# Performance work log

Measured on AMD Instinct MI355X. Metric: run time of the kernel, lower is better.

Reference implementation:

```python
import jax, jax.numpy as jnp
import numpy as np
from jax import lax

B, S, H, I, E, K = 4, 4096, 1024, 3584, 8, 2


def setup_inputs() -> dict:
    key = jax.random.key(0)
    ks = jax.random.split(key, 5)
    scale_h = 1.0 / np.sqrt(H)
    scale_i = 1.0 / np.sqrt(I)
    return {
        "hidden_states": jax.random.normal(ks[0], (B, S, H), dtype=jnp.float32),
        "gate_w": jax.random.normal(ks[1], (E, H), dtype=jnp.float32) * scale_h,
        "w1": jax.random.normal(ks[2], (E, H, I), dtype=jnp.float32) * scale_h,
        "w3": jax.random.normal(ks[3], (E, H, I), dtype=jnp.float32) * scale_h,
        "w2": jax.random.normal(ks[4], (E, I, H), dtype=jnp.float32) * scale_i,
        "top_k": K,
    }


def reference(hidden_states, gate_w, w1, w3, w2, top_k):
    b, s, h = hidden_states.shape
    n_experts = gate_w.shape[0]
    x = hidden_states.reshape(-1, h)  # [T, H]

    # Router: softmax in fp32, top-k, renormalize (Mixtral style)
    logits = x @ gate_w.T  # [T, E]
    probs = jax.nn.softmax(logits.astype(jnp.float32), axis=-1)
    top_w, top_idx = lax.top_k(probs, top_k)  # [T, K]
    top_w = top_w.astype(x.dtype)
    top_w = top_w / jnp.sum(top_w, axis=-1, keepdims=True)

    # Per-token, per-expert combine weight: [T, E]
    one_hot = jax.nn.one_hot(top_idx, n_experts, dtype=x.dtype)  # [T, K, E]
    w_full = jnp.einsum("tk,tke->te", top_w, one_hot)

    out = jnp.zeros_like(x)
    for e in range(n_experts):  # fixed small loop over experts
        hidden = jax.nn.silu(x @ w1[e]) * (x @ w3[e])  # SwiGLU, [T, I]
        y = hidden @ w2[e]  # [T, H]
        out = out + y * w_full[:, e:e + 1]
    return out.reshape(b, s, h)
```

## Files before the change

kernel.cpp:

```cpp
#include <hip/hip_runtime.h>
#include <hip/hip_bf16.h>

#define T_TOK 16384
#define H_DIM 1024
#define I_DIM 3584
#define E_NUM 8
#define TOTP  32768

typedef __attribute__((ext_vector_type(8))) short s16x8;
typedef __attribute__((ext_vector_type(4))) float f32x4;
typedef unsigned short u16;

__device__ __forceinline__ u16 f2bf(float f) {
    union { float f; unsigned u; } c; c.f = f;
    unsigned r = c.u + 0x7fffu + ((c.u >> 16) & 1u);
    return (u16)(r >> 16);
}

__device__ __forceinline__ void glds16(const u16* g, u16* l) {
    __builtin_amdgcn_global_load_lds(
        (const __attribute__((address_space(1))) unsigned int*)g,
        (__attribute__((address_space(3))) unsigned int*)l,
        16, 0, 0);
}

__global__ __launch_bounds__(64)
void router_k(const float* __restrict__ x, const float* __restrict__ gw,
              int* __restrict__ tk_idx, float* __restrict__ tk_w,
              int* __restrict__ counts, u16* __restrict__ xb)
{
    int t = blockIdx.x;
    int lane = threadIdx.x;
    const float* xr = x + (size_t)t * H_DIM;
    float xv[16];
#pragma unroll
    for (int j = 0; j < 16; j++) xv[j] = xr[j * 64 + lane];
    u16* xo = xb + (size_t)t * H_DIM;
#pragma unroll
    for (int j = 0; j < 16; j++) xo[j * 64 + lane] = f2bf(xv[j]);
    float lg[E_NUM];
#pragma unroll
    for (int e = 0; e < E_NUM; e++) {
        const float* g = gw + e * H_DIM;
        float s = 0.f;
#pragma unroll
        for (int j = 0; j < 16; j++) s += xv[j] * g[j * 64 + lane];
#pragma unroll
        for (int off = 32; off > 0; off >>= 1) s += __shfl_xor(s, off, 64);
        lg[e] = s;
    }
    if (lane == 0) {
        int i1 = 0; float m1 = lg[0];
#pragma unroll
        for (int e = 1; e < E_NUM; e++) if (lg[e] > m1) { m1 = lg[e]; i1 = e; }
        int i2 = -1; float m2 = -3.4e38f;
#pragma unroll
        for (int e = 0; e < E_NUM; e++) if (e != i1 && lg[e] > m2) { m2 = lg[e]; i2 = e; }
        float p1 = 1.f / (1.f + __expf(m2 - m1));
        float p2 = 1.f - p1;
        tk_idx[t * 2]     = i1;
        tk_idx[t * 2 + 1] = i2;
        tk_w[t * 2]       = p1;
        tk_w[t * 2 + 1]   = p2;
        atomicAdd(&counts[i1], 1);
        atomicAdd(&counts[i2], 1);
    }
}

__global__ void offsets_k(const int* __restrict__ counts, int* __restrict__ offsets,
                          int* __restrict__ cursor)
{
    if (threadIdx.x == 0 && blockIdx.x == 0) {
        int acc = 0;
        for (int e = 0; e < E_NUM; e++) { offsets[e] = acc; cursor[e] = acc; acc += counts[e]; }
        offsets[E_NUM] = acc;
    }
}

__global__ __launch_bounds__(256)
void scatter_k(const int* __restrict__ tk_idx, const float* __restrict__ tk_w,
               int* __restrict__ cursor, int* __restrict__ perm, float* __restrict__ pw,
               int* __restrict__ posmap)
{
    int t = blockIdx.x * 256 + threadIdx.x;
    if (t >= T_TOK) return;
#pragma unroll
    for (int k = 0; k < 2; k++) {
        int e = tk_idx[t * 2 + k];
        int pos = atomicAdd(&cursor[e], 1);
        perm[pos] = t;
        pw[pos]   = tk_w[t * 2 + k];
        posmap[t * 2 + k] = pos;
    }
}

__global__ __launch_bounds__(256)
void tcvt_k(const float* __restrict__ src, u16* __restrict__ dst, int M, int N)
{
    size_t eo = (size_t)blockIdx.z * M * N;
    __shared__ u16 tl[32][33];
    int t = threadIdx.x;
    int r = t >> 3, c = (t & 7) * 4;
    int m0 = blockIdx.y * 32, n0 = blockIdx.x * 32;
    float4 v = *reinterpret_cast<const float4*>(src + eo + (size_t)(m0 + r) * N + n0 + c);
    tl[c + 0][r] = f2bf(v.x); tl[c + 1][r] = f2bf(v.y);
    tl[c + 2][r] = f2bf(v.z); tl[c + 3][r] = f2bf(v.w);
    __syncthreads();
    union { u16 s[4]; unsigned long long v; } u;
    u.s[0] = tl[r][c]; u.s[1] = tl[r][c + 1]; u.s[2] = tl[r][c + 2]; u.s[3] = tl[r][c + 3];
    *reinterpret_cast<unsigned long long*>(dst + eo + (size_t)(n0 + r) * M + m0 + c) = u.v;
}

__global__ __launch_bounds__(256, 2)
void gemm1_k(const u16* __restrict__ xb, const u16* __restrict__ w1t,
             const u16* __restrict__ w3t, const int* __restrict__ offsets,
             const int* __restrict__ perm, const float* __restrict__ pw,
             u16* __restrict__ hidden)
{
    int e = blockIdx.z;
    int base = offsets[e];
    int cnt  = offsets[e + 1] - base;
    int m0 = blockIdx.y * 128;
    if (m0 >= cnt) return;
    int n0 = blockIdx.x * 64;

    __shared__ u16 As[128 * 32];
    __shared__ u16 B1s[64 * 32];
    __shared__ u16 B3s[64 * 32];

    int t = threadIdx.x;
    int lane = t & 63, wave = t >> 6;
    int wm = (wave >> 1) * 64, wn = (wave & 1) * 32;
    int l15 = lane & 15, quad = lane >> 4;

    int sr = t >> 2;
    int sc = (t & 3) * 8;
    int p0 = m0 + sr;      if (p0 > cnt - 1) p0 = cnt - 1;
    int p1 = m0 + 64 + sr; if (p1 > cnt - 1) p1 = cnt - 1;
    const u16* a0p = xb + (size_t)perm[base + p0] * H_DIM + sc;
    const u16* a1p = xb + (size_t)perm[base + p1] * H_DIM + sc;
    const u16* b1p = w1t + (size_t)e * I_DIM * H_DIM + (size_t)(n0 + sr) * H_DIM + sc;
    const u16* b3p = w3t + (size_t)e * I_DIM * H_DIM + (size_t)(n0 + sr) * H_DIM + sc;

    u16* As0 = As + t * 8;
    u16* As1 = As + 2048 + t * 8;
    u16* B1d = B1s + t * 8;
    u16* B3d = B3s + t * 8;

    f32x4 acc1[4][2] = {};
    f32x4 acc3[4][2] = {};

    for (int k0 = 0; k0 < H_DIM; k0 += 32) {
        glds16(a0p + k0, As0);
        glds16(a1p + k0, As1);
        glds16(b1p + k0, B1d);
        glds16(b3p + k0, B3d);
        __syncthreads();
        s16x8 af[4];
#pragma unroll
        for (int i = 0; i < 4; i++)
            af[i] = *reinterpret_cast<const s16x8*>(As + (wm + i * 16 + l15) * 32 + quad * 8);
#pragma unroll
        for (int j = 0; j < 2; j++) {
            s16x8 b1 = *reinterpret_cast<const s16x8*>(B1s + (wn + j * 16 + l15) * 32 + quad * 8);
            s16x8 b3 = *reinterpret_cast<const s16x8*>(B3s + (wn + j * 16 + l15) * 32 + quad * 8);
#pragma unroll
            for (int i = 0; i < 4; i++) {
                acc1[i][j] = __builtin_amdgcn_mfma_f32_16x16x32_bf16(af[i], b1, acc1[i][j], 0, 0, 0);
                acc3[i][j] = __builtin_amdgcn_mfma_f32_16x16x32_bf16(af[i], b3, acc3[i][j], 0, 0, 0);
            }
        }
        __syncthreads();
    }

#pragma unroll
    for (int i = 0; i < 4; i++) {
#pragma unroll
        for (int j = 0; j < 2; j++) {
            int col = n0 + wn + j * 16 + l15;
#pragma unroll
            for (int r = 0; r < 4; r++) {
                int p = m0 + wm + i * 16 + quad * 4 + r;
                if (p < cnt) {
                    float z1 = acc1[i][j][r];
                    float z3 = acc3[i][j][r];
                    float hv = (z1 / (1.f + __expf(-z1))) * z3 * pw[base + p];
                    hidden[(size_t)(base + p) * I_DIM + col] = f2bf(hv);
                }
            }
        }
    }
}

__global__ __launch_bounds__(256, 2)
void gemm2_k(const u16* __restrict__ hidden, const u16* __restrict__ w2t,
             const int* __restrict__ offsets, float* __restrict__ ybuf)
{
    int e = blockIdx.z;
    int base = offsets[e];
    int cnt  = offsets[e + 1] - base;
    int m0 = blockIdx.y * 128;
    if (m0 >= cnt) return;
    int n0 = blockIdx.x * 128;

    __shared__ u16 As[128 * 32];
    __shared__ u16 Bs[128 * 32];

    int t = threadIdx.x;
    int lane = t & 63, wave = t >> 6;
    int wm = (wave >> 1) * 64, wn = (wave & 1) * 64;
    int l15 = lane & 15, quad = lane >> 4;

    int sr = t >> 2;
    int sc = (t & 3) * 8;
    int p0 = m0 + sr;      if (p0 > cnt - 1) p0 = cnt - 1;
    int p1 = m0 + 64 + sr; if (p1 > cnt - 1) p1 = cnt - 1;
    const u16* a0p = hidden + (size_t)(base + p0) * I_DIM + sc;
    const u16* a1p = hidden + (size_t)(base + p1) * I_DIM + sc;
    const u16* wb  = w2t + (size_t)e * H_DIM * I_DIM;
    const u16* b0p = wb + (size_t)(n0 + sr) * I_DIM + sc;
    const u16* b1p = wb + (size_t)(n0 + 64 + sr) * I_DIM + sc;

    u16* As0 = As + t * 8;
    u16* As1 = As + 2048 + t * 8;
    u16* Bs0 = Bs + t * 8;
    u16* Bs1 = Bs + 2048 + t * 8;

    f32x4 acc[4][4] = {};

    for (int k0 = 0; k0 < I_DIM; k0 += 32) {
        glds16(a0p + k0, As0);
        glds16(a1p + k0, As1);
        glds16(b0p + k0, Bs0);
        glds16(b1p + k0, Bs1);
        __syncthreads();
        s16x8 af[4];
#pragma unroll
        for (int i = 0; i < 4; i++)
            af[i] = *reinterpret_cast<const s16x8*>(As + (wm + i * 16 + l15) * 32 + quad * 8);
#pragma unroll
        for (int j = 0; j < 4; j++) {
            s16x8 bfv = *reinterpret_cast<const s16x8*>(Bs + (wn + j * 16 + l15) * 32 + quad * 8);
#pragma unroll
            for (int i = 0; i < 4; i++)
                acc[i][j] = __builtin_amdgcn_mfma_f32_16x16x32_bf16(af[i], bfv, acc[i][j], 0, 0, 0);
        }
        __syncthreads();
    }

#pragma unroll
    for (int i = 0; i < 4; i++) {
#pragma unroll
        for (int r = 0; r < 4; r++) {
            int p = m0 + wm + i * 16 + quad * 4 + r;
            if (p < cnt) {
                float* orow = ybuf + (size_t)(base + p) * H_DIM + n0 + wn;
#pragma unroll
                for (int j = 0; j < 4; j++)
                    orow[j * 16 + l15] = acc[i][j][r];
            }
        }
    }
}

__global__ __launch_bounds__(256)
void combine_k(const float* __restrict__ ybuf, const int* __restrict__ posmap,
               float* __restrict__ out)
{
    int t = blockIdx.x;
    int c = threadIdx.x * 4;
    int pa = posmap[t * 2];
    int pb = posmap[t * 2 + 1];
    float4 a = *reinterpret_cast<const float4*>(ybuf + (size_t)pa * H_DIM + c);
    float4 b = *reinterpret_cast<const float4*>(ybuf + (size_t)pb * H_DIM + c);
    float4 o = make_float4(a.x + b.x, a.y + b.y, a.z + b.z, a.w + b.w);
    *reinterpret_cast<float4*>(out + (size_t)t * H_DIM + c) = o;
}

extern "C" void kernel_launch(void* const* d_in, const int* in_sizes, int n_in,
                              void* d_out, int out_size, void* d_ws, size_t ws_size,
                              hipStream_t stream)
{
    (void)in_sizes; (void)n_in; (void)ws_size; (void)out_size;
    const float* x  = (const float*)d_in[0];
    const float* gw = (const float*)d_in[1];
    const float* w1 = (const float*)d_in[2];
    const float* w3 = (const float*)d_in[3];
    const float* w2 = (const float*)d_in[4];
    float* out = (float*)d_out;

    char* ws = (char*)d_ws;
    int*   counts  = (int*)ws;
    int*   offsets = counts + 8;
    int*   cursor  = offsets + 9;
    int*   tk_idx  = (int*)(ws + 128);
    float* tk_w    = (float*)(ws + 128 + 131072);
    int*   perm    = (int*)(ws + 128 + 2 * 131072);
    float* pw      = (float*)(ws + 128 + 3 * 131072);
    int*   posmap  = (int*)(ws + 128 + 4 * 131072);
    u16* xb     = (u16*)(ws + (1 << 20));
    u16* w1t    = xb + 16777216ull;
    u16* w3t    = w1t + 29360128ull;
    u16* w2t    = w3t + 29360128ull;
    u16* hidden = w2t + 29360128ull;
    float* ybuf = (float*)(ws + (1 << 20));

    hipMemsetAsync(ws, 0, 128, stream);
    router_k<<<T_TOK, 64, 0, stream>>>(x, gw, tk_idx, tk_w, counts, xb);
    offsets_k<<<1, 64, 0, stream>>>(counts, offsets, cursor);
    scatter_k<<<T_TOK / 256, 256, 0, stream>>>(tk_idx, tk_w, cursor, perm, pw, posmap);
    tcvt_k<<<dim3(I_DIM / 32, H_DIM / 32, E_NUM), 256, 0, stream>>>(w1, w1t, H_DIM, I_DIM);
    tcvt_k<<<dim3(I_DIM / 32, H_DIM / 32, E_NUM), 256, 0, stream>>>(w3, w3t, H_DIM, I_DIM);
    tcvt_k<<<dim3(H_DIM / 32, I_DIM / 32, E_NUM), 256, 0, stream>>>(w2, w2t, I_DIM, H_DIM);
    gemm1_k<<<dim3(I_DIM / 64, 128, E_NUM), 256, 0, stream>>>(xb, w1t, w3t, offsets, perm, pw, hidden);
    gemm2_k<<<dim3(H_DIM / 128, 128, E_NUM), 256, 0, stream>>>(hidden, w2t, offsets, ybuf);
    combine_k<<<T_TOK, 256, 0, stream>>>(ybuf, posmap, out);
}
```

Before: 1.906 ms.

## Enlarge GEMM tiles to 256x256x64 with double-buffered LDS, swizzle and interleaved w1/w3

Both expert GEMMs move from 128-row tiles with 32-wide K steps to 256x256 tiles with 64-wide K steps and 512 threads. LDS is double-buffered so the next K tile's global-to-LDS loads overlap the MFMAs, with XOR-swizzled LDS addressing and s_setprio around the MFMA blocks. w1 and w3 are packed into one interleaved transposed matrix, so gemm1 reads a single B operand whose adjacent 16-column groups hold matching gate and up outputs. This is meant to raise arithmetic intensity and hide load latency, at the cost of 128KB LDS per block, many more accumulator registers, and more wasted work on the last partial row tile of each expert.

```diff
diff --git a/kernel.cpp b/kernel.cpp
--- a/kernel.cpp
+++ b/kernel.cpp
@@ -5,6 +5,7 @@
 #define H_DIM 1024
 #define I_DIM 3584
 #define E_NUM 8
+#define N13   7168
 #define TOTP  32768
 
 typedef __attribute__((ext_vector_type(8))) short s16x8;
@@ -111,153 +112,244 @@
     *reinterpret_cast<unsigned long long*>(dst + eo + (size_t)(n0 + r) * M + m0 + c) = u.v;
 }
 
-__global__ __launch_bounds__(256, 2)
-void gemm1_k(const u16* __restrict__ xb, const u16* __restrict__ w1t,
-             const u16* __restrict__ w3t, const int* __restrict__ offsets,
-             const int* __restrict__ perm, const float* __restrict__ pw,
-             u16* __restrict__ hidden)
+__global__ __launch_bounds__(256)
+void tcvt13_k(const float* __restrict__ src, u16* __restrict__ dst, int mat)
+{
+    size_t eo_s = (size_t)blockIdx.z * H_DIM * I_DIM;
+    size_t eo_d = (size_t)blockIdx.z * (size_t)N13 * H_DIM;
+    __shared__ u16 tl[32][33];
+    int t = threadIdx.x;
+    int r = t >> 3, c = (t & 7) * 4;
+    int m0 = blockIdx.y * 32, n0 = blockIdx.x * 32;
+    float4 v = *reinterpret_cast<const float4*>(src + eo_s + (size_t)(m0 + r) * I_DIM + n0 + c);
+    tl[c + 0][r] = f2bf(v.x); tl[c + 1][r] = f2bf(v.y);
+    tl[c + 2][r] = f2bf(v.z); tl[c + 3][r] = f2bf(v.w);
+    __syncthreads();
+    union { u16 s[4]; unsigned long long v; } u;
+    u.s[0] = tl[r][c]; u.s[1] = tl[r][c + 1]; u.s[2] = tl[r][c + 2]; u.s[3] = tl[r][c + 3];
+    int ic = n0 + r;
+    int orow = ((ic >> 4) << 5) + (mat << 4) + (ic & 15);
+    *reinterpret_cast<unsigned long long*>(dst + eo_d + (size_t)orow * H_DIM + m0 + c) = u.v;
+}
+
+
+__global__ __launch_bounds__(512, 2)
+void gemm1_k(const u16* __restrict__ xb, const u16* __restrict__ w13t,
+             const int* __restrict__ offsets, const int* __restrict__ perm,
+             const float* __restrict__ pw, u16* __restrict__ hidden)
 {
     int e = blockIdx.z;
     int base = offsets[e];
     int cnt  = offsets[e + 1] - base;
-    int m0 = blockIdx.y * 128;
+    int m0 = blockIdx.y * 256;
     if (m0 >= cnt) return;
-    int n0 = blockIdx.x * 64;
-
-    __shared__ u16 As[128 * 32];
-    __shared__ u16 B1s[64 * 32];
-    __shared__ u16 B3s[64 * 32];
+    int n0 = blockIdx.x * 256;
+
+    __shared__ u16 As[2][256 * 64];
+    __shared__ u16 Bs[2][256 * 64];
 
     int t = threadIdx.x;
     int lane = t & 63, wave = t >> 6;
-    int wm = (wave >> 1) * 64, wn = (wave & 1) * 32;
+    int wm = (wave >> 2) * 128;
+    int wn = (wave & 3) * 64;
     int l15 = lane & 15, quad = lane >> 4;
-
-    int sr = t >> 2;
-    int sc = (t & 3) * 8;
-    int p0 = m0 + sr;      if (p0 > cnt - 1) p0 = cnt - 1;
-    int p1 = m0 + 64 + sr; if (p1 > cnt - 1) p1 = cnt - 1;
-    const u16* a0p = xb + (size_t)perm[base + p0] * H_DIM + sc;
-    const u16* a1p = xb + (size_t)perm[base + p1] * H_DIM + sc;
-    const u16* b1p = w1t + (size_t)e * I_DIM * H_DIM + (size_t)(n0 + sr) * H_DIM + sc;
-    const u16* b3p = w3t + (size_t)e * I_DIM * H_DIM + (size_t)(n0 + sr) * H_DIM + sc;
-
-    u16* As0 = As + t * 8;
-    u16* As1 = As + 2048 + t * 8;
-    u16* B1d = B1s + t * 8;
-    u16* B3d = B3s + t * 8;
-
-    f32x4 acc1[4][2] = {};
-    f32x4 acc3[4][2] = {};
-
-    for (int k0 = 0; k0 < H_DIM; k0 += 32) {
-        glds16(a0p + k0, As0);
-        glds16(a1p + k0, As1);
-        glds16(b1p + k0, B1d);
-        glds16(b3p + k0, B3d);
-        __syncthreads();
-        s16x8 af[4];
-#pragma unroll
-        for (int i = 0; i < 4; i++)
-            af[i] = *reinterpret_cast<const s16x8*>(As + (wm + i * 16 + l15) * 32 + quad * 8);
-#pragma unroll
-        for (int j = 0; j < 2; j++) {
-            s16x8 b1 = *reinterpret_cast<const s16x8*>(B1s + (wn + j * 16 + l15) * 32 + quad * 8);
-            s16x8 b3 = *reinterpret_cast<const s16x8*>(B3s + (wn + j * 16 + l15) * 32 + quad * 8);
+    int x7 = l15 & 7;
+    int s0 = (quad ^ x7) * 8;
+    int s1 = ((4 + quad) ^ x7) * 8;
+
+    int sr = t >> 3;
+    int ss = t & 7;
+    const u16* aptr[4];
+    const u16* bptr[4];
+#pragma unroll
+    for (int l = 0; l < 4; l++) {
+        int ra = l * 64 + sr;
+        int pr = m0 + ra; if (pr > cnt - 1) pr = cnt - 1;
+        aptr[l] = xb + (size_t)perm[base + pr] * H_DIM + (ss ^ (ra & 7)) * 8;
+        bptr[l] = w13t + (size_t)e * N13 * H_DIM + (size_t)(n0 + ra) * H_DIM + (ss ^ (ra & 7)) * 8;
+    }
+
+    auto STAGE = [&](int buf, int k0) {
+#pragma unroll
+        for (int l = 0; l < 4; l++) glds16(aptr[l] + k0, &As[buf][l * 4096 + t * 8]);
+#pragma unroll
+        for (int l = 0; l < 4; l++) glds16(bptr[l] + k0, &Bs[buf][l * 4096 + t * 8]);
+    };
+
+    f32x4 acc[8][4] = {};
+    const int NT = H_DIM / 64;
+
+    STAGE(0, 0);
+    for (int kt = 0; kt < NT; ++kt) {
+        int cur = kt & 1;
+        if (kt + 1 < NT) {
+            STAGE(cur ^ 1, (kt + 1) * 64);
+            asm volatile("s_waitcnt vmcnt(8)" ::: "memory");
+        } else {
+            asm volatile("s_waitcnt vmcnt(0)" ::: "memory");
+        }
+        __builtin_amdgcn_s_barrier();
+        asm volatile("" ::: "memory");
+        const u16* Ab = As[cur];
+        const u16* Bb = Bs[cur];
+#pragma unroll
+        for (int mh = 0; mh < 2; mh++)
+#pragma unroll
+        for (int nh = 0; nh < 2; nh++) {
+            s16x8 af[4][2], bf[2][2];
 #pragma unroll
             for (int i = 0; i < 4; i++) {
-                acc1[i][j] = __builtin_amdgcn_mfma_f32_16x16x32_bf16(af[i], b1, acc1[i][j], 0, 0, 0);
-                acc3[i][j] = __builtin_amdgcn_mfma_f32_16x16x32_bf16(af[i], b3, acc3[i][j], 0, 0, 0);
-            }
-        }
-        __syncthreads();
-    }
-
-#pragma unroll
-    for (int i = 0; i < 4; i++) {
-#pragma unroll
-        for (int j = 0; j < 2; j++) {
-            int col = n0 + wn + j * 16 + l15;
-#pragma unroll
-            for (int r = 0; r < 4; r++) {
-                int p = m0 + wm + i * 16 + quad * 4 + r;
-                if (p < cnt) {
-                    float z1 = acc1[i][j][r];
-                    float z3 = acc3[i][j][r];
-                    float hv = (z1 / (1.f + __expf(-z1))) * z3 * pw[base + p];
-                    hidden[(size_t)(base + p) * I_DIM + col] = f2bf(hv);
+                int row = wm + mh * 64 + i * 16 + l15;
+                af[i][0] = *reinterpret_cast<const s16x8*>(Ab + row * 64 + s0);
+                af[i][1] = *reinterpret_cast<const s16x8*>(Ab + row * 64 + s1);
+            }
+#pragma unroll
+            for (int j = 0; j < 2; j++) {
+                int row = wn + nh * 32 + j * 16 + l15;
+                bf[j][0] = *reinterpret_cast<const s16x8*>(Bb + row * 64 + s0);
+                bf[j][1] = *reinterpret_cast<const s16x8*>(Bb + row * 64 + s1);
+            }
+            __builtin_amdgcn_s_setprio(1);
+#pragma unroll
+            for (int j = 0; j < 2; j++)
+#pragma unroll
+            for (int i = 0; i < 4; i++)
+#pragma unroll
+            for (int kk = 0; kk < 2; kk++)
+                acc[mh * 4 + i][nh * 2 + j] = __builtin_amdgcn_mfma_f32_16x16x32_bf16(
+                    af[i][kk], bf[j][kk], acc[mh * 4 + i][nh * 2 + j], 0, 0, 0);
+            __builtin_amdgcn_s_setprio(0);
+        }
+        __builtin_amdgcn_s_barrier();
+        asm volatile("" ::: "memory");
+    }
+
+    int hc0 = (n0 + wn) >> 1;
+#pragma unroll
+    for (int i = 0; i < 8; i++) {
+        int rowoff = (i >> 2) * 64 + (i & 3) * 16 + quad * 4;
+#pragma unroll
+        for (int r = 0; r < 4; r++) {
+            int p = m0 + wm + rowoff + r;
+            if (p < cnt) {
+                float w = pw[base + p];
+                u16* hrow = hidden + (size_t)(base + p) * I_DIM + hc0;
+#pragma unroll
+                for (int nh = 0; nh < 2; nh++) {
+                    float z1 = acc[i][nh * 2 + 0][r];
+                    float z3 = acc[i][nh * 2 + 1][r];
+                    float hv = (z1 / (1.f + __expf(-z1))) * z3 * w;
+                    hrow[nh * 16 + l15] = f2bf(hv);
                 }
             }
         }
     }
 }
 
-__global__ __launch_bounds__(256, 2)
+__global__ __launch_bounds__(512, 2)
 void gemm2_k(const u16* __restrict__ hidden, const u16* __restrict__ w2t,
              const int* __restrict__ offsets, float* __restrict__ ybuf)
 {
     int e = blockIdx.z;
     int base = offsets[e];
     int cnt  = offsets[e + 1] - base;
-    int m0 = blockIdx.y * 128;
+    int m0 = blockIdx.y * 256;
     if (m0 >= cnt) return;
-    int n0 = blockIdx.x * 128;
-
-    __shared__ u16 As[128 * 32];
-    __shared__ u16 Bs[128 * 32];
+    int n0 = blockIdx.x * 256;
+
+    __shared__ u16 As[2][256 * 64];
+    __shared__ u16 Bs[2][256 * 64];
 
     int t = threadIdx.x;
     int lane = t & 63, wave = t >> 6;
-    int wm = (wave >> 1) * 64, wn = (wave & 1) * 64;
+    int wm = (wave >> 2) * 128;
+    int wn = (wave & 3) * 64;
     int l15 = lane & 15, quad = lane >> 4;
-
-    int sr = t >> 2;
-    int sc = (t & 3) * 8;
-    int p0 = m0 + sr;      if (p0 > cnt - 1) p0 = cnt - 1;
-    int p1 = m0 + 64 + sr; if (p1 > cnt - 1) p1 = cnt - 1;
-    const u16* a0p = hidden + (size_t)(base + p0) * I_DIM + sc;
-    const u16* a1p = hidden + (size_t)(base + p1) * I_DIM + sc;
-    const u16* wb  = w2t + (size_t)e * H_DIM * I_DIM;
-    const u16* b0p = wb + (size_t)(n0 + sr) * I_DIM + sc;
-    const u16* b1p = wb + (size_t)(n0 + 64 + sr) * I_DIM + sc;
-
-    u16* As0 = As + t * 8;
-    u16* As1 = As + 2048 + t * 8;
-    u16* Bs0 = Bs + t * 8;
-    u16* Bs1 = Bs + 2048 + t * 8;
-
-    f32x4 acc[4][4] = {};
-
-    for (int k0 = 0; k0 < I_DIM; k0 += 32) {
-        glds16(a0p + k0, As0);
-        glds16(a1p + k0, As1);
-        glds16(b0p + k0, Bs0);
-        glds16(b1p + k0, Bs1);
-        __syncthreads();
-        s16x8 af[4];
-#pragma unroll
-        for (int i = 0; i < 4; i++)
-            af[i] = *reinterpret_cast<const s16x8*>(As + (wm + i * 16 + l15) * 32 + quad * 8);
-#pragma unroll
-        for (int j = 0; j < 4; j++) {
-            s16x8 bfv = *reinterpret_cast<const s16x8*>(Bs + (wn + j * 16 + l15) * 32 + quad * 8);
+    int x7 = l15 & 7;
+    int s0 = (quad ^ x7) * 8;
+    int s1 = ((4 + quad) ^ x7) * 8;
+
+    int sr = t >> 3;
+    int ss = t & 7;
+    const u16* aptr[4];
+    const u16* bptr[4];
+    const u16* wb = w2t + (size_t)e * H_DIM * I_DIM;
+#pragma unroll
+    for (int l = 0; l < 4; l++) {
+        int ra = l * 64 + sr;
+        int pr = m0 + ra; if (pr > cnt - 1) pr = cnt - 1;
+        aptr[l] = hidden + (size_t)(base + pr) * I_DIM + (ss ^ (ra & 7)) * 8;
+        bptr[l] = wb + (size_t)(n0 + ra) * I_DIM + (ss ^ (ra & 7)) * 8;
+    }
+
+    auto STAGE = [&](int buf, int k0) {
+#pragma unroll
+        for (int l = 0; l < 4; l++) glds16(aptr[l] + k0, &As[buf][l * 4096 + t * 8]);
+#pragma unroll
+        for (int l = 0; l < 4; l++) glds16(bptr[l] + k0, &Bs[buf][l * 4096 + t * 8]);
+    };
+
+    f32x4 acc[8][4] = {};
+    const int NT = I_DIM / 64;
+
+    STAGE(0, 0);
+    for (int kt = 0; kt < NT; ++kt) {
+        int cur = kt & 1;
+        if (kt + 1 < NT) {
+            STAGE(cur ^ 1, (kt + 1) * 64);
+            asm volatile("s_waitcnt vmcnt(8)" ::: "memory");
+        } else {
+            asm volatile("s_waitcnt vmcnt(0)" ::: "memory");
+        }
+        __builtin_amdgcn_s_barrier();
+        asm volatile("" ::: "memory");
+        const u16* Ab = As[cur];
+        const u16* Bb = Bs[cur];
+#pragma unroll
+        for (int mh = 0; mh < 2; mh++)
+#pragma unroll
+        for (int nh = 0; nh < 2; nh++) {
+            s16x8 af[4][2], bf[2][2];
+#pragma unroll
+            for (int i = 0; i < 4; i++) {
+                int row = wm + mh * 64 + i * 16 + l15;
+                af[i][0] = *reinterpret_cast<const s16x8*>(Ab + row * 64 + s0);
+                af[i][1] = *reinterpret_cast<const s16x8*>(Ab + row * 64 + s1);
+            }
+#pragma unroll
+            for (int j = 0; j < 2; j++) {
+                int row = wn + nh * 32 + j * 16 + l15;
+                bf[j][0] = *reinterpret_cast<const s16x8*>(Bb + row * 64 + s0);
+                bf[j][1] = *reinterpret_cast<const s16x8*>(Bb + row * 64 + s1);
+            }
+            __builtin_amdgcn_s_setprio(1);
+#pragma unroll
+            for (int j = 0; j < 2; j++)
 #pragma unroll
             for (int i = 0; i < 4; i++)
-                acc[i][j] = __builtin_amdgcn_mfma_f32_16x16x32_bf16(af[i], bfv, acc[i][j], 0, 0, 0);
-        }
-        __syncthreads();
-    }
-
-#pragma unroll
-    for (int i = 0; i < 4; i++) {
+#pragma unroll
+            for (int kk = 0; kk < 2; kk++)
+                acc[mh * 4 + i][nh * 2 + j] = __builtin_amdgcn_mfma_f32_16x16x32_bf16(
+                    af[i][kk], bf[j][kk], acc[mh * 4 + i][nh * 2 + j], 0, 0, 0);
+            __builtin_amdgcn_s_setprio(0);
+        }
+        __builtin_amdgcn_s_barrier();
+        asm volatile("" ::: "memory");
+    }
+
+#pragma unroll
+    for (int i = 0; i < 8; i++) {
+        int rowoff = (i >> 2) * 64 + (i & 3) * 16 + quad * 4;
 #pragma unroll
         for (int r = 0; r < 4; r++) {
-            int p = m0 + wm + i * 16 + quad * 4 + r;
+            int p = m0 + wm + rowoff + r;
             if (p < cnt) {
                 float* orow = ybuf + (size_t)(base + p) * H_DIM + n0 + wn;
 #pragma unroll
-                for (int j = 0; j < 4; j++)
-                    orow[j * 16 + l15] = acc[i][j][r];
+                for (int nh = 0; nh < 2; nh++)
+#pragma unroll
+                for (int j = 0; j < 2; j++)
+                    orow[nh * 32 + j * 16 + l15] = acc[i][nh * 2 + j][r];
             }
         }
     }
@@ -299,9 +391,8 @@
     float* pw      = (float*)(ws + 128 + 3 * 131072);
     int*   posmap  = (int*)(ws + 128 + 4 * 131072);
     u16* xb     = (u16*)(ws + (1 << 20));
-    u16* w1t    = xb + 16777216ull;
-    u16* w3t    = w1t + 29360128ull;
-    u16* w2t    = w3t + 29360128ull;
+    u16* w13t   = xb + 16777216ull;
+    u16* w2t    = w13t + 58720256ull;
     u16* hidden = w2t + 29360128ull;
     float* ybuf = (float*)(ws + (1 << 20));
 
@@ -309,10 +400,10 @@
     router_k<<<T_TOK, 64, 0, stream>>>(x, gw, tk_idx, tk_w, counts, xb);
     offsets_k<<<1, 64, 0, stream>>>(counts, offsets, cursor);
     scatter_k<<<T_TOK / 256, 256, 0, stream>>>(tk_idx, tk_w, cursor, perm, pw, posmap);
-    tcvt_k<<<dim3(I_DIM / 32, H_DIM / 32, E_NUM), 256, 0, stream>>>(w1, w1t, H_DIM, I_DIM);
-    tcvt_k<<<dim3(I_DIM / 32, H_DIM / 32, E_NUM), 256, 0, stream>>>(w3, w3t, H_DIM, I_DIM);
+    tcvt13_k<<<dim3(I_DIM / 32, H_DIM / 32, E_NUM), 256, 0, stream>>>(w1, w13t, 0);
+    tcvt13_k<<<dim3(I_DIM / 32, H_DIM / 32, E_NUM), 256, 0, stream>>>(w3, w13t, 1);
     tcvt_k<<<dim3(H_DIM / 32, I_DIM / 32, E_NUM), 256, 0, stream>>>(w2, w2t, I_DIM, H_DIM);
-    gemm1_k<<<dim3(I_DIM / 64, 128, E_NUM), 256, 0, stream>>>(xb, w1t, w3t, offsets, perm, pw, hidden);
-    gemm2_k<<<dim3(H_DIM / 128, 128, E_NUM), 256, 0, stream>>>(hidden, w2t, offsets, ybuf);
+    gemm1_k<<<dim3(N13 / 256, 64, E_NUM), 512, 0, stream>>>(xb, w13t, offsets, perm, pw, hidden);
+    gemm2_k<<<dim3(H_DIM / 256, 64, E_NUM), 512, 0, stream>>>(hidden, w2t, offsets, ybuf);
     combine_k<<<T_TOK, 256, 0, stream>>>(ybuf, posmap, out);
 }
```

Result: slower. 1.989 ms (+4.3%).
